# Optimization experiments

Hardware: AMD Instinct MI355X
Metric: run time of the kernel (lower is better)

Reference implementation:

```python
import jax, jax.numpy as jnp
import numpy as np

IN_DIM = 768
NUM_TAGS = 50
NC = NUM_TAGS + 2  # tags + START + END
START = NUM_TAGS
END = NUM_TAGS + 1
NEG = -1000000000.0


def setup_inputs() -> dict:
    key = jax.random.key(0)
    k1, k2, k3, k4, k5, k6 = jax.random.split(key, 6)
    B, L = 64, 512
    x = jax.random.normal(k1, (B, L, IN_DIM), dtype=jnp.float32)
    y = jax.random.randint(k2, (B, L), 0, NUM_TAGS)
    lengths = jax.random.randint(k3, (B,), 1, L + 1)
    # linear projection params (in_dim != num_tags)
    W = jax.random.normal(k4, (NUM_TAGS, IN_DIM), dtype=jnp.float32) * (1.0 / np.sqrt(IN_DIM))
    b = jnp.zeros((NUM_TAGS,), dtype=jnp.float32)
    # transition matrix: xavier-normal then forbid transitions into START and out of END
    T = jax.random.normal(k5, (NC, NC), dtype=jnp.float32) * np.sqrt(2.0 / (NC + NC))
    T = T.at[:, START].set(NEG)
    T = T.at[END, :].set(NEG)
    return {"x": x, "y": y, "lengths": lengths, "W": W, "b": b, "T": T}


def _crf_nll(x, y, lengths, W, b, T):
    B, L, H = x.shape
    lengths = jnp.maximum(lengths, 1)
    mask = jnp.arange(L)[None, :] < lengths[:, None]  # [B,L] bool, contiguous prefix
    mf = mask.astype(x.dtype)
    # linear projection + mask + append START/END emit scores
    logits = (jnp.einsum('blh,th->blt', x, W) + b) * mf[:, :, None]  # [B,L,num_tags]
    xe = jnp.concatenate([logits, jnp.full((B, L, 2), NEG, logits.dtype)], axis=-1)  # [B,L,NC]

    # ---- forward algorithm (logsumexp scan over time) ----
    alpha0 = jnp.full((B, NC), NEG, xe.dtype).at[:, START].set(0.0)

    def step(alpha, inp):
        e_t, m_t = inp  # [B,NC], [B]
        scores = alpha[:, :, None] + T[None, :, :] + e_t[:, None, :]  # [B,NC,NC]
        new = jax.scipy.special.logsumexp(scores, axis=1)
        alpha = jnp.where(m_t[:, None], new, alpha)
        return alpha, None

    alpha, _ = jax.lax.scan(step, alpha0, (xe.transpose(1, 0, 2), mask.T))
    all_path_score = jax.scipy.special.logsumexp(alpha + T[:, END][None, :], axis=-1)  # [B]

    # ---- gold path score (vectorized version of the per-step loop) ----
    emit = jnp.take_along_axis(xe, y[:, :, None], axis=-1)[:, :, 0]  # [B,L]
    path = T[START, y[:, 0]]
    path = path + jnp.sum(emit[:, : L - 1] * mf[:, : L - 1], axis=-1)
    path = path + jnp.sum(T[y[:, : L - 1], y[:, 1:]] * mf[:, 1:], axis=-1)
    real_last_tag = y[jnp.arange(B), lengths - 1]  # [B]
    emit_last = jnp.take_along_axis(xe[:, -1], real_last_tag[:, None], axis=1)[:, 0] * mf[:, -1]
    path = path + emit_last + T[real_last_tag, END]

    return jnp.mean(all_path_score - path)


def reference(x, y, lengths, W, b, T):
    return _crf_nll(x, y, lengths, W, b, T)
```

## Files before the change

### kernel.cpp

```cpp
#include <hip/hip_runtime.h>
#include <hip/hip_bf16.h>
#include <cstdint>

#define IN_DIMX 768
#define NTAGS 50
#define NCC 52
#define LSEQ 512
#define BATCH 64
#define START_TAG 50
#define END_TAG 51
#define NEGV (-1000000000.0f)
#define LOG2E 1.4426950408889634f
#define LN2 0.6931471805599453f

#define BM 64
#define BN 64
#define BKC 64
#define LDSP (BM + 4)

__global__ __launch_bounds__(256) void gemm_logits(
    const float* __restrict__ x, const float* __restrict__ W,
    const float* __restrict__ bias, float* __restrict__ outL)
{
  __shared__ float xs[BKC][LDSP];
  __shared__ float ws[BKC][LDSP];
  const int tid = threadIdx.x;
  const int bx = blockIdx.x;
  const size_t row0 = (size_t)bx * BM;
  const int ty = tid >> 4, tx = tid & 15;
  const int lr = tid >> 4, lk = tid & 15;
  float acc[4][4] = {};

  for (int kc = 0; kc < IN_DIMX; kc += BKC) {
    #pragma unroll
    for (int rr = 0; rr < 4; ++rr) {
      const int r = lr + rr * 16;
      const float4 v = *reinterpret_cast<const float4*>(&x[(row0 + r) * IN_DIMX + kc + lk * 4]);
      xs[lk*4+0][r] = v.x; xs[lk*4+1][r] = v.y; xs[lk*4+2][r] = v.z; xs[lk*4+3][r] = v.w;
    }
    #pragma unroll
    for (int rr = 0; rr < 4; ++rr) {
      const int c = lr + rr * 16;
      float4 v = make_float4(0.f, 0.f, 0.f, 0.f);
      if (c < NTAGS) v = *reinterpret_cast<const float4*>(&W[c * IN_DIMX + kc + lk * 4]);
      ws[lk*4+0][c] = v.x; ws[lk*4+1][c] = v.y; ws[lk*4+2][c] = v.z; ws[lk*4+3][c] = v.w;
    }
    __syncthreads();
    #pragma unroll
    for (int kk = 0; kk < BKC; ++kk) {
      const float4 a  = *reinterpret_cast<const float4*>(&xs[kk][ty * 4]);
      const float4 bq = *reinterpret_cast<const float4*>(&ws[kk][tx * 4]);
      acc[0][0] += a.x*bq.x; acc[0][1] += a.x*bq.y; acc[0][2] += a.x*bq.z; acc[0][3] += a.x*bq.w;
      acc[1][0] += a.y*bq.x; acc[1][1] += a.y*bq.y; acc[1][2] += a.y*bq.z; acc[1][3] += a.y*bq.w;
      acc[2][0] += a.z*bq.x; acc[2][1] += a.z*bq.y; acc[2][2] += a.z*bq.z; acc[2][3] += a.z*bq.w;
      acc[3][0] += a.w*bq.x; acc[3][1] += a.w*bq.y; acc[3][2] += a.w*bq.z; acc[3][3] += a.w*bq.w;
    }
    __syncthreads();
  }
  #pragma unroll
  for (int i = 0; i < 4; ++i) {
    const int r = ty * 4 + i;
    const int c = tx * 4;
    float4 o;
    o.x = acc[i][0] + ((c + 0) < NTAGS ? bias[c + 0] : 0.f);
    o.y = acc[i][1] + ((c + 1) < NTAGS ? bias[c + 1] : 0.f);
    o.z = acc[i][2] + ((c + 2) < NTAGS ? bias[c + 2] : 0.f);
    o.w = acc[i][3] + ((c + 3) < NTAGS ? bias[c + 3] : 0.f);
    *reinterpret_cast<float4*>(&outL[(row0 + r) * 64 + c]) = o;
  }
}

__device__ __forceinline__ float lane_bcast(float v, int lane) {
  return __int_as_float(__builtin_amdgcn_readlane(__float_as_int(v), lane));
}

__global__ __launch_bounds__(64) void crf_scan(
    const float* __restrict__ logits, const int* __restrict__ y,
    const int* __restrict__ lengths, const float* __restrict__ T,
    float* __restrict__ out)
{
  const int b = blockIdx.x;
  const int j = threadIdx.x;
  const int jj = (j < NCC) ? j : (NCC - 1);
  const bool act = (j < NCC);
  const bool emit = (j < NTAGS);

  float E[NCC];
  #pragma unroll
  for (int i = 0; i < NCC; ++i) {
    const float tv = T[i * NCC + jj];
    E[i] = act ? exp2f(tv * LOG2E) : 0.f;
  }
  const float E2 = act ? exp2f(T[jj * NCC + END_TAG] * LOG2E) : 0.f;

  int len = lengths[b]; if (len < 1) len = 1;
  const float* lrow = logits + (size_t)b * LSEQ * 64;

  float p  = (j == START_TAG) ? 1.f : 0.f;
  float Mc = 0.f;
  float r  = 1.f;
  float sCur = emit ? exp2f(lrow[j] * LOG2E) : 0.f;

  for (int t = 0; t < len; ++t) {
    const int tn = (t + 1 < len) ? (t + 1) : t;
    const float eN = emit ? lrow[tn * 64 + j] : 0.f;
    const float scale = sCur * r;

    float q0 = 0.f, q1 = 0.f, q2 = 0.f, q3 = 0.f;
    #pragma unroll
    for (int i = 0; i < NCC; i += 4) {
      q0 = fmaf(lane_bcast(p, i + 0), E[i + 0], q0);
      q1 = fmaf(lane_bcast(p, i + 1), E[i + 1], q1);
      q2 = fmaf(lane_bcast(p, i + 2), E[i + 2], q2);
      q3 = fmaf(lane_bcast(p, i + 3), E[i + 3], q3);
    }
    const float q = (q0 + q1) + (q2 + q3);
    p = q * scale;

    Mc -= log2f(r);
    const float p0 = lane_bcast(p, 0);
    r = 1.0f / p0;
    sCur = emit ? exp2f(eN * LOG2E) : 0.f;
  }

  float v = p * E2;
  #pragma unroll
  for (int off = 32; off; off >>= 1) v += __shfl_xor(v, off, 64);
  const float all_path = (Mc + log2f(v)) * LN2;

  const int* yb = y + b * LSEQ;
  float ps = 0.f;
  for (int t = j; t < len; t += 64) {
    const int yt = yb[t];
    ps += lrow[t * 64 + yt];
    if (t >= 1) ps += T[yb[t - 1] * NCC + yt];
  }
  #pragma unroll
  for (int off = 32; off; off >>= 1) ps += __shfl_xor(ps, off, 64);

  if (j == 0) {
    const float path = ps + T[START_TAG * NCC + yb[0]]
                     + T[yb[len - 1] * NCC + END_TAG];
    atomicAdd(out, (all_path - path) * (1.0f / BATCH));
  }
}

__global__ void zero_out_k(float* o) { o[0] = 0.f; }

extern "C" void kernel_launch(void* const* d_in, const int* in_sizes, int n_in,
                              void* d_out, int out_size, void* d_ws, size_t ws_size,
                              hipStream_t stream) {
  const float* x       = (const float*)d_in[0];
  const int*   y       = (const int*)d_in[1];
  const int*   lengths = (const int*)d_in[2];
  const float* W       = (const float*)d_in[3];
  const float* bias    = (const float*)d_in[4];
  const float* T       = (const float*)d_in[5];
  float* outp   = (float*)d_out;
  float* logits = (float*)d_ws;

  zero_out_k<<<1, 1, 0, stream>>>(outp);
  gemm_logits<<<(BATCH * LSEQ) / BM, 256, 0, stream>>>(x, W, bias, logits);
  crf_scan<<<BATCH, 64, 0, stream>>>(logits, y, lengths, T, outp);
}
```

Measured before the change: 463.3 us.

## Register-prefetch GEMM with swizzled LDS and trim CRF scan recurrence

The logits GEMM now runs 128 threads per block, each computing 8x4 outputs. It prefetches the next K chunk of x and W into registers while computing the current one, and XOR-swizzles LDS columns to reduce bank conflicts. In the CRF scan, the first timestep is peeled using the START-row transitions. The sum skips the START/END rows, which only hold zero probability, and the division is replaced by a hardware reciprocal. These changes aim to hide global-load latency in the memory-bound GEMM and shorten the serial per-step dependency chain, at the cost of more registers, lower thread count per block and a slightly less accurate reciprocal.

```diff
diff --git a/kernel.cpp b/kernel.cpp
--- a/kernel.cpp
+++ b/kernel.cpp
@@ -13,53 +13,94 @@
 #define LOG2E 1.4426950408889634f
 #define LN2 0.6931471805599453f
 
-#define BM 64
-#define BN 64
-#define BKC 64
-#define LDSP (BM + 4)
-
-__global__ __launch_bounds__(256) void gemm_logits(
+#define GBM 64
+#define GBK 64
+#define GLDSP 68
+#define NKC (IN_DIMX / GBK)
+
+__global__ __launch_bounds__(128) void gemm_logits(
     const float* __restrict__ x, const float* __restrict__ W,
     const float* __restrict__ bias, float* __restrict__ outL)
 {
-  __shared__ float xs[BKC][LDSP];
-  __shared__ float ws[BKC][LDSP];
+  __shared__ float xs[GBK][GLDSP];
+  __shared__ float ws[GBK][GLDSP];
   const int tid = threadIdx.x;
-  const int bx = blockIdx.x;
-  const size_t row0 = (size_t)bx * BM;
-  const int ty = tid >> 4, tx = tid & 15;
-  const int lr = tid >> 4, lk = tid & 15;
-  float acc[4][4] = {};
-
-  for (int kc = 0; kc < IN_DIMX; kc += BKC) {
+  const size_t row0 = (size_t)blockIdx.x * GBM;
+  const int ty = tid >> 4;
+  const int tx = tid & 15;
+  const int lr = tid >> 4;
+  const int lk = tid & 15;
+  const int sw = (lk & 7) << 2;
+
+  float acc[8][4] = {};
+  float4 xr[8], wr[8];
+
+#define LOADCHUNK(KC)                                                          \
+  {                                                                            \
+    const int kb = (KC) * GBK + lk * 4;                                        \
+    _Pragma("unroll")                                                          \
+    for (int rr = 0; rr < 8; ++rr) {                                           \
+      const int r = lr + rr * 8;                                               \
+      xr[rr] = *reinterpret_cast<const float4*>(&x[(row0 + r) * IN_DIMX + kb]);\
+    }                                                                          \
+    _Pragma("unroll")                                                          \
+    for (int rr = 0; rr < 8; ++rr) {                                           \
+      const int c = lr + rr * 8;                                               \
+      wr[rr] = (c < NTAGS)                                                     \
+          ? *reinterpret_cast<const float4*>(&W[c * IN_DIMX + kb])             \
+          : make_float4(0.f, 0.f, 0.f, 0.f);                                   \
+    }                                                                          \
+  }
+
+#define STORECHUNK()                                                           \
+  {                                                                            \
+    _Pragma("unroll")                                                          \
+    for (int rr = 0; rr < 8; ++rr) {                                           \
+      const int r = (lr + rr * 8) ^ sw;                                        \
+      xs[lk * 4 + 0][r] = xr[rr].x;                                            \
+      xs[lk * 4 + 1][r] = xr[rr].y;                                            \
+      xs[lk * 4 + 2][r] = xr[rr].z;                                            \
+      xs[lk * 4 + 3][r] = xr[rr].w;                                            \
+      ws[lk * 4 + 0][r] = wr[rr].x;                                            \
+      ws[lk * 4 + 1][r] = wr[rr].y;                                            \
+      ws[lk * 4 + 2][r] = wr[rr].z;                                            \
+      ws[lk * 4 + 3][r] = wr[rr].w;                                            \
+    }                                                                          \
+  }
+
+  LOADCHUNK(0)
+  STORECHUNK()
+  __syncthreads();
+
+  for (int kc = 0; kc < NKC; ++kc) {
+    if (kc + 1 < NKC) LOADCHUNK(kc + 1)
+
     #pragma unroll
-    for (int rr = 0; rr < 4; ++rr) {
-      const int r = lr + rr * 16;
-      const float4 v = *reinterpret_cast<const float4*>(&x[(row0 + r) * IN_DIMX + kc + lk * 4]);
-      xs[lk*4+0][r] = v.x; xs[lk*4+1][r] = v.y; xs[lk*4+2][r] = v.z; xs[lk*4+3][r] = v.w;
+    for (int kk = 0; kk < GBK; ++kk) {
+      const int s4 = ((kk >> 2) & 7) << 2;
+      const float4 a0 = *reinterpret_cast<const float4*>(&xs[kk][(ty * 8 + 0) ^ s4]);
+      const float4 a1 = *reinterpret_cast<const float4*>(&xs[kk][(ty * 8 + 4) ^ s4]);
+      const float4 bq = *reinterpret_cast<const float4*>(&ws[kk][(tx * 4) ^ s4]);
+      acc[0][0] += a0.x*bq.x; acc[0][1] += a0.x*bq.y; acc[0][2] += a0.x*bq.z; acc[0][3] += a0.x*bq.w;
+      acc[1][0] += a0.y*bq.x; acc[1][1] += a0.y*bq.y; acc[1][2] += a0.y*bq.z; acc[1][3] += a0.y*bq.w;
+      acc[2][0] += a0.z*bq.x; acc[2][1] += a0.z*bq.y; acc[2][2] += a0.z*bq.z; acc[2][3] += a0.z*bq.w;
+      acc[3][0] += a0.w*bq.x; acc[3][1] += a0.w*bq.y; acc[3][2] += a0.w*bq.z; acc[3][3] += a0.w*bq.w;
+      acc[4][0] += a1.x*bq.x; acc[4][1] += a1.x*bq.y; acc[4][2] += a1.x*bq.z; acc[4][3] += a1.x*bq.w;
+      acc[5][0] += a1.y*bq.x; acc[5][1] += a1.y*bq.y; acc[5][2] += a1.y*bq.z; acc[5][3] += a1.y*bq.w;
+      acc[6][0] += a1.z*bq.x; acc[6][1] += a1.z*bq.y; acc[6][2] += a1.z*bq.z; acc[6][3] += a1.z*bq.w;
+      acc[7][0] += a1.w*bq.x; acc[7][1] += a1.w*bq.y; acc[7][2] += a1.w*bq.z; acc[7][3] += a1.w*bq.w;
     }
-    #pragma unroll
-    for (int rr = 0; rr < 4; ++rr) {
-      const int c = lr + rr * 16;
-      float4 v = make_float4(0.f, 0.f, 0.f, 0.f);
-      if (c < NTAGS) v = *reinterpret_cast<const float4*>(&W[c * IN_DIMX + kc + lk * 4]);
-      ws[lk*4+0][c] = v.x; ws[lk*4+1][c] = v.y; ws[lk*4+2][c] = v.z; ws[lk*4+3][c] = v.w;
+
+    if (kc + 1 < NKC) {
+      __syncthreads();
+      STORECHUNK()
+      __syncthreads();
     }
-    __syncthreads();
-    #pragma unroll
-    for (int kk = 0; kk < BKC; ++kk) {
-      const float4 a  = *reinterpret_cast<const float4*>(&xs[kk][ty * 4]);
-      const float4 bq = *reinterpret_cast<const float4*>(&ws[kk][tx * 4]);
-      acc[0][0] += a.x*bq.x; acc[0][1] += a.x*bq.y; acc[0][2] += a.x*bq.z; acc[0][3] += a.x*bq.w;
-      acc[1][0] += a.y*bq.x; acc[1][1] += a.y*bq.y; acc[1][2] += a.y*bq.z; acc[1][3] += a.y*bq.w;
-      acc[2][0] += a.z*bq.x; acc[2][1] += a.z*bq.y; acc[2][2] += a.z*bq.z; acc[2][3] += a.z*bq.w;
-      acc[3][0] += a.w*bq.x; acc[3][1] += a.w*bq.y; acc[3][2] += a.w*bq.z; acc[3][3] += a.w*bq.w;
-    }
-    __syncthreads();
-  }
+  }
+
   #pragma unroll
-  for (int i = 0; i < 4; ++i) {
-    const int r = ty * 4 + i;
+  for (int i = 0; i < 8; ++i) {
+    const int r = ty * 8 + i;
     const int c = tx * 4;
     float4 o;
     o.x = acc[i][0] + ((c + 0) < NTAGS ? bias[c + 0] : 0.f);
@@ -73,6 +114,12 @@
 __device__ __forceinline__ float lane_bcast(float v, int lane) {
   return __int_as_float(__builtin_amdgcn_readlane(__float_as_int(v), lane));
 }
+
+#define LA(X) X(0) X(4) X(8) X(12) X(16) X(20) X(24) X(28) X(32) X(36) X(40) X(44) X(48)
+#define LB(X) X(1) X(5) X(9) X(13) X(17) X(21) X(25) X(29) X(33) X(37) X(41) X(45) X(49)
+#define LC(X) X(2) X(6) X(10) X(14) X(18) X(22) X(26) X(30) X(34) X(38) X(42) X(46)
+#define LD(X) X(3) X(7) X(11) X(15) X(19) X(23) X(27) X(31) X(35) X(39) X(43) X(47)
+#define L50(X) LA(X) LB(X) LC(X) LD(X)
 
 __global__ __launch_bounds__(64) void crf_scan(
     const float* __restrict__ logits, const int* __restrict__ y,
@@ -85,42 +132,39 @@
   const bool act = (j < NCC);
   const bool emit = (j < NTAGS);
 
-  float E[NCC];
-  #pragma unroll
-  for (int i = 0; i < NCC; ++i) {
-    const float tv = T[i * NCC + jj];
-    E[i] = act ? exp2f(tv * LOG2E) : 0.f;
-  }
-  const float E2 = act ? exp2f(T[jj * NCC + END_TAG] * LOG2E) : 0.f;
+  #define DECLE(i) const float e##i = act ? exp2f(T[(i) * NCC + jj] * LOG2E) : 0.f;
+  L50(DECLE)
+  const float eStart = act ? exp2f(T[START_TAG * NCC + jj] * LOG2E) : 0.f;
+  const float E2     = act ? exp2f(T[jj * NCC + END_TAG] * LOG2E) : 0.f;
 
   int len = lengths[b]; if (len < 1) len = 1;
   const float* lrow = logits + (size_t)b * LSEQ * 64;
 
-  float p  = (j == START_TAG) ? 1.f : 0.f;
+  float sCur = emit ? exp2f(lrow[j] * LOG2E) : 0.f;
+  float p  = eStart * sCur;
   float Mc = 0.f;
-  float r  = 1.f;
-  float sCur = emit ? exp2f(lrow[j] * LOG2E) : 0.f;
-
-  for (int t = 0; t < len; ++t) {
+  float r  = __builtin_amdgcn_rcpf(lane_bcast(p, 0));
+  float eN = (emit && 1 < len) ? lrow[64 + j] : 0.f;
+
+  for (int t = 1; t < len; ++t) {
+    const float scale = (emit ? exp2f(eN * LOG2E) : 0.f) * r;
     const int tn = (t + 1 < len) ? (t + 1) : t;
-    const float eN = emit ? lrow[tn * 64 + j] : 0.f;
-    const float scale = sCur * r;
-
-    float q0 = 0.f, q1 = 0.f, q2 = 0.f, q3 = 0.f;
-    #pragma unroll
-    for (int i = 0; i < NCC; i += 4) {
-      q0 = fmaf(lane_bcast(p, i + 0), E[i + 0], q0);
-      q1 = fmaf(lane_bcast(p, i + 1), E[i + 1], q1);
-      q2 = fmaf(lane_bcast(p, i + 2), E[i + 2], q2);
-      q3 = fmaf(lane_bcast(p, i + 3), E[i + 3], q3);
-    }
-    const float q = (q0 + q1) + (q2 + q3);
+    eN = emit ? lrow[tn * 64 + j] : 0.f;
+
+    float qa = 0.f, qb = 0.f, qc = 0.f, qd = 0.f;
+    #define FMA_A(i) qa = fmaf(lane_bcast(p, i), e##i, qa);
+    #define FMA_B(i) qb = fmaf(lane_bcast(p, i), e##i, qb);
+    #define FMA_C(i) qc = fmaf(lane_bcast(p, i), e##i, qc);
+    #define FMA_D(i) qd = fmaf(lane_bcast(p, i), e##i, qd);
+    LA(FMA_A)
+    LB(FMA_B)
+    LC(FMA_C)
+    LD(FMA_D)
+    const float q = (qa + qb) + (qc + qd);
+
+    Mc -= log2f(r);
     p = q * scale;
-
-    Mc -= log2f(r);
-    const float p0 = lane_bcast(p, 0);
-    r = 1.0f / p0;
-    sCur = emit ? exp2f(eN * LOG2E) : 0.f;
+    r = __builtin_amdgcn_rcpf(lane_bcast(p, 0));
   }
 
   float v = p * E2;
@@ -160,6 +204,6 @@
   float* logits = (float*)d_ws;
 
   zero_out_k<<<1, 1, 0, stream>>>(outp);
-  gemm_logits<<<(BATCH * LSEQ) / BM, 256, 0, stream>>>(x, W, bias, logits);
+  gemm_logits<<<(BATCH * LSEQ) / GBM, 128, 0, stream>>>(x, W, bias, logits);
   crf_scan<<<BATCH, 64, 0, stream>>>(logits, y, lengths, T, outp);
 }
```

Result: slower. 989.2 us (+113.5%).

## Rewrite logits GEMM with register-held W and double-buffered x; trim CRF scan

Applied to the files above, without the earlier changes.

The projection GEMM now gives each lane one tag column, holds that column's W slice in registers per chunk, and double-buffers x tiles in LDS so the next chunk's global loads overlap compute. The CRF scan drops the START/END rows from the recurrence, since their alpha is zero after step one. It also unrolls time by four with rotating emission prefetch registers and uses the hardware reciprocal instead of a division. This aims to cut global-load latency in the serial scan and improve GEMM load overlap, at the cost of more register pressure and redundant W loads per block.

```diff
diff --git a/kernel.cpp b/kernel.cpp
--- a/kernel.cpp
+++ b/kernel.cpp
@@ -13,66 +13,91 @@
 #define LOG2E 1.4426950408889634f
 #define LN2 0.6931471805599453f
 
-#define BM 64
-#define BN 64
-#define BKC 64
-#define LDSP (BM + 4)
+#define NKC (IN_DIMX / 64)
 
 __global__ __launch_bounds__(256) void gemm_logits(
     const float* __restrict__ x, const float* __restrict__ W,
     const float* __restrict__ bias, float* __restrict__ outL)
 {
-  __shared__ float xs[BKC][LDSP];
-  __shared__ float ws[BKC][LDSP];
+  __shared__ __align__(16) float xls[2][64][64];
   const int tid = threadIdx.x;
-  const int bx = blockIdx.x;
-  const size_t row0 = (size_t)bx * BM;
-  const int ty = tid >> 4, tx = tid & 15;
-  const int lr = tid >> 4, lk = tid & 15;
-  float acc[4][4] = {};
+  const int wid = tid >> 6;
+  const int j   = tid & 63;
+  const size_t row0 = (size_t)blockIdx.x * 64;
+  const bool wcol = (j < NTAGS);
+  const float biasv = wcol ? bias[j] : 0.f;
 
-  for (int kc = 0; kc < IN_DIMX; kc += BKC) {
-    #pragma unroll
-    for (int rr = 0; rr < 4; ++rr) {
-      const int r = lr + rr * 16;
-      const float4 v = *reinterpret_cast<const float4*>(&x[(row0 + r) * IN_DIMX + kc + lk * 4]);
-      xs[lk*4+0][r] = v.x; xs[lk*4+1][r] = v.y; xs[lk*4+2][r] = v.z; xs[lk*4+3][r] = v.w;
-    }
-    #pragma unroll
-    for (int rr = 0; rr < 4; ++rr) {
-      const int c = lr + rr * 16;
-      float4 v = make_float4(0.f, 0.f, 0.f, 0.f);
-      if (c < NTAGS) v = *reinterpret_cast<const float4*>(&W[c * IN_DIMX + kc + lk * 4]);
-      ws[lk*4+0][c] = v.x; ws[lk*4+1][c] = v.y; ws[lk*4+2][c] = v.z; ws[lk*4+3][c] = v.w;
-    }
-    __syncthreads();
-    #pragma unroll
-    for (int kk = 0; kk < BKC; ++kk) {
-      const float4 a  = *reinterpret_cast<const float4*>(&xs[kk][ty * 4]);
-      const float4 bq = *reinterpret_cast<const float4*>(&ws[kk][tx * 4]);
-      acc[0][0] += a.x*bq.x; acc[0][1] += a.x*bq.y; acc[0][2] += a.x*bq.z; acc[0][3] += a.x*bq.w;
-      acc[1][0] += a.y*bq.x; acc[1][1] += a.y*bq.y; acc[1][2] += a.y*bq.z; acc[1][3] += a.y*bq.w;
-      acc[2][0] += a.z*bq.x; acc[2][1] += a.z*bq.y; acc[2][2] += a.z*bq.z; acc[2][3] += a.z*bq.w;
-      acc[3][0] += a.w*bq.x; acc[3][1] += a.w*bq.y; acc[3][2] += a.w*bq.z; acc[3][3] += a.w*bq.w;
-    }
-    __syncthreads();
+  float4 xr[4];
+  float4 wv[16];
+  float  acc[16];
+  #pragma unroll
+  for (int r = 0; r < 16; ++r) acc[r] = 0.f;
+
+  #pragma unroll
+  for (int it = 0; it < 4; ++it) {
+    const int O = it * 256 + tid;
+    xr[it] = *reinterpret_cast<const float4*>(
+        &x[(row0 + (O >> 4)) * IN_DIMX + (O & 15) * 4]);
   }
   #pragma unroll
-  for (int i = 0; i < 4; ++i) {
-    const int r = ty * 4 + i;
-    const int c = tx * 4;
-    float4 o;
-    o.x = acc[i][0] + ((c + 0) < NTAGS ? bias[c + 0] : 0.f);
-    o.y = acc[i][1] + ((c + 1) < NTAGS ? bias[c + 1] : 0.f);
-    o.z = acc[i][2] + ((c + 2) < NTAGS ? bias[c + 2] : 0.f);
-    o.w = acc[i][3] + ((c + 3) < NTAGS ? bias[c + 3] : 0.f);
-    *reinterpret_cast<float4*>(&outL[(row0 + r) * 64 + c]) = o;
+  for (int it = 0; it < 4; ++it) {
+    const int O = it * 256 + tid;
+    *reinterpret_cast<float4*>(&xls[0][O >> 4][(O & 15) * 4]) = xr[it];
   }
+
+  for (int c = 0; c < NKC; ++c) {
+    #pragma unroll
+    for (int kq = 0; kq < 16; ++kq)
+      wv[kq] = wcol ? *reinterpret_cast<const float4*>(
+                          &W[j * IN_DIMX + c * 64 + kq * 4])
+                    : make_float4(0.f, 0.f, 0.f, 0.f);
+    const int cn = (c + 1 < NKC) ? c + 1 : NKC - 1;
+    #pragma unroll
+    for (int it = 0; it < 4; ++it) {
+      const int O = it * 256 + tid;
+      xr[it] = *reinterpret_cast<const float4*>(
+          &x[(row0 + (O >> 4)) * IN_DIMX + cn * 64 + (O & 15) * 4]);
+    }
+
+    __syncthreads();
+
+    const float (*xb)[64] = xls[c & 1];
+    const int rbase = wid * 16;
+    #pragma unroll
+    for (int r = 0; r < 16; ++r) {
+      float q0 = 0.f, q1 = 0.f, q2 = 0.f, q3 = 0.f;
+      #pragma unroll
+      for (int kq = 0; kq < 16; ++kq) {
+        const float4 xv = *reinterpret_cast<const float4*>(&xb[rbase + r][kq * 4]);
+        q0 = fmaf(xv.x, wv[kq].x, q0);
+        q1 = fmaf(xv.y, wv[kq].y, q1);
+        q2 = fmaf(xv.z, wv[kq].z, q2);
+        q3 = fmaf(xv.w, wv[kq].w, q3);
+      }
+      acc[r] += (q0 + q1) + (q2 + q3);
+    }
+
+    #pragma unroll
+    for (int it = 0; it < 4; ++it) {
+      const int O = it * 256 + tid;
+      *reinterpret_cast<float4*>(&xls[(c + 1) & 1][O >> 4][(O & 15) * 4]) = xr[it];
+    }
+  }
+
+  #pragma unroll
+  for (int r = 0; r < 16; ++r)
+    outL[(row0 + wid * 16 + r) * 64 + j] = acc[r] + biasv;
 }
 
 __device__ __forceinline__ float lane_bcast(float v, int lane) {
   return __int_as_float(__builtin_amdgcn_readlane(__float_as_int(v), lane));
 }
+
+#define LA(X) X(0) X(4) X(8) X(12) X(16) X(20) X(24) X(28) X(32) X(36) X(40) X(44) X(48)
+#define LB(X) X(1) X(5) X(9) X(13) X(17) X(21) X(25) X(29) X(33) X(37) X(41) X(45) X(49)
+#define LC(X) X(2) X(6) X(10) X(14) X(18) X(22) X(26) X(30) X(34) X(38) X(42) X(46)
+#define LD(X) X(3) X(7) X(11) X(15) X(19) X(23) X(27) X(31) X(35) X(39) X(43) X(47)
+#define L50(X) LA(X) LB(X) LC(X) LD(X)
 
 __global__ __launch_bounds__(64) void crf_scan(
     const float* __restrict__ logits, const int* __restrict__ y,
@@ -85,43 +110,51 @@
   const bool act = (j < NCC);
   const bool emit = (j < NTAGS);
 
-  float E[NCC];
-  #pragma unroll
-  for (int i = 0; i < NCC; ++i) {
-    const float tv = T[i * NCC + jj];
-    E[i] = act ? exp2f(tv * LOG2E) : 0.f;
-  }
-  const float E2 = act ? exp2f(T[jj * NCC + END_TAG] * LOG2E) : 0.f;
+  #define DECLE(i) const float e##i = act ? exp2f(T[(i) * NCC + jj] * LOG2E) : 0.f;
+  L50(DECLE)
+  const float eStart = act ? exp2f(T[START_TAG * NCC + jj] * LOG2E) : 0.f;
+  const float E2     = act ? exp2f(T[jj * NCC + END_TAG] * LOG2E) : 0.f;
 
   int len = lengths[b]; if (len < 1) len = 1;
   const float* lrow = logits + (size_t)b * LSEQ * 64;
 
-  float p  = (j == START_TAG) ? 1.f : 0.f;
+  float p  = eStart * (emit ? exp2f(lrow[j] * LOG2E) : 0.f);
   float Mc = 0.f;
-  float r  = 1.f;
-  float sCur = emit ? exp2f(lrow[j] * LOG2E) : 0.f;
+  float r  = __builtin_amdgcn_rcpf(lane_bcast(p, 0));
 
-  for (int t = 0; t < len; ++t) {
-    const int tn = (t + 1 < len) ? (t + 1) : t;
-    const float eN = emit ? lrow[tn * 64 + j] : 0.f;
-    const float scale = sCur * r;
+  float eA = emit ? lrow[1 * 64 + j] : 0.f;
+  float eB = emit ? lrow[2 * 64 + j] : 0.f;
+  float eC = emit ? lrow[3 * 64 + j] : 0.f;
+  float eD = emit ? lrow[4 * 64 + j] : 0.f;
 
-    float q0 = 0.f, q1 = 0.f, q2 = 0.f, q3 = 0.f;
-    #pragma unroll
-    for (int i = 0; i < NCC; i += 4) {
-      q0 = fmaf(lane_bcast(p, i + 0), E[i + 0], q0);
-      q1 = fmaf(lane_bcast(p, i + 1), E[i + 1], q1);
-      q2 = fmaf(lane_bcast(p, i + 2), E[i + 2], q2);
-      q3 = fmaf(lane_bcast(p, i + 3), E[i + 3], q3);
-    }
-    const float q = (q0 + q1) + (q2 + q3);
-    p = q * scale;
+  #define FMA_A(i) qa = fmaf(lane_bcast(p, i), e##i, qa);
+  #define FMA_B(i) qb = fmaf(lane_bcast(p, i), e##i, qb);
+  #define FMA_C(i) qc = fmaf(lane_bcast(p, i), e##i, qc);
+  #define FMA_D(i) qd = fmaf(lane_bcast(p, i), e##i, qd);
 
-    Mc -= log2f(r);
-    const float p0 = lane_bcast(p, 0);
-    r = 1.0f / p0;
-    sCur = emit ? exp2f(eN * LOG2E) : 0.f;
+  #define STEPX(EREG, TT)                                                     \
+  {                                                                           \
+    const float scale = (emit ? exp2f((EREG) * LOG2E) : 0.f) * r;             \
+    int tl = (TT) + 4; tl = (tl > LSEQ - 1) ? (LSEQ - 1) : tl;                \
+    EREG = emit ? lrow[tl * 64 + j] : 0.f;                \
+    float qa = 0.f, qb = 0.f, qc = 0.f, qd = 0.f;                             \
+    LA(FMA_A) LB(FMA_B) LC(FMA_C) LD(FMA_D)                                   \
+    const float q = (qa + qb) + (qc + qd);                                    \
+    Mc -= log2f(r);                                                           \
+    p = q * scale;                                                            \
+    r = __builtin_amdgcn_rcpf(lane_bcast(p, 0));                              \
   }
+
+  int t = 1;
+  for (; t + 3 < len; t += 4) {
+    STEPX(eA, t)
+    STEPX(eB, t + 1)
+    STEPX(eC, t + 2)
+    STEPX(eD, t + 3)
+  }
+  if (t     < len) STEPX(eA, t)
+  if (t + 1 < len) STEPX(eB, t + 1)
+  if (t + 2 < len) STEPX(eC, t + 2)
 
   float v = p * E2;
   #pragma unroll
@@ -130,10 +163,10 @@
 
   const int* yb = y + b * LSEQ;
   float ps = 0.f;
-  for (int t = j; t < len; t += 64) {
-    const int yt = yb[t];
-    ps += lrow[t * 64 + yt];
-    if (t >= 1) ps += T[yb[t - 1] * NCC + yt];
+  for (int tt = j; tt < len; tt += 64) {
+    const int yt = yb[tt];
+    ps += lrow[tt * 64 + yt];
+    if (tt >= 1) ps += T[yb[tt - 1] * NCC + yt];
   }
   #pragma unroll
   for (int off = 32; off; off >>= 1) ps += __shfl_xor(ps, off, 64);
@@ -160,6 +193,6 @@
   float* logits = (float*)d_ws;
 
   zero_out_k<<<1, 1, 0, stream>>>(outp);
-  gemm_logits<<<(BATCH * LSEQ) / BM, 256, 0, stream>>>(x, W, bias, logits);
+  gemm_logits<<<(BATCH * LSEQ) / 64, 256, 0, stream>>>(x, W, bias, logits);
   crf_scan<<<BATCH, 64, 0, stream>>>(logits, y, lengths, T, outp);
 }
```

New measurement: 482.5 us. +4.1%, slower.
